# Kernel optimization log

Hardware: AMD Instinct MI355X
Metric: run time of the kernel (lower is better)

Reference implementation:

```python
import jax, jax.numpy as jnp
import numpy as np

H = 1024   # hidden_size
S = 1024   # seq_length
B = 32     # batch_size


def setup_inputs() -> dict:
    key = jax.random.key(0)
    k1, k2, k3, k4, k5, k6 = jax.random.split(key, 6)
    scale = 1.0 / np.sqrt(3 * H)
    return {
        "encoder_states": jax.random.normal(k1, (S, B, 2 * H), dtype=jnp.float32),
        "hidden": jax.random.normal(k2, (B, H), dtype=jnp.float32),
        "cell": jax.random.normal(k3, (B, H), dtype=jnp.float32),
        "W_attn": jax.random.normal(k4, (H, 3 * H), dtype=jnp.float32) * scale,
        "b_attn": jax.random.normal(k5, (H,), dtype=jnp.float32) * scale,
        "v_w": jax.random.normal(k6, (H,), dtype=jnp.float32) * (1.0 / np.sqrt(H)),
    }


def reference(encoder_states, hidden, cell, W_attn, b_attn, v_w):
    # cell is accepted by the original forward but unused.
    # Split the concat-linear into two projections (mathematically identical,
    # avoids materializing the repeated hidden + concat tensor):
    # cat((hidden_rep, enc), -1) @ W.T == hidden @ W[:, :H].T + enc @ W[:, H:].T
    W_h = W_attn[:, :H]          # [H, H]   multiplies decoder hidden
    W_e = W_attn[:, H:]          # [H, 2H]  multiplies encoder states
    enc = jnp.transpose(encoder_states, (1, 0, 2))          # [B, S, 2H]
    h_proj = hidden @ W_h.T + b_attn                         # [B, H], broadcast over S
    e_proj = jnp.einsum("bse,he->bsh", enc, W_e)             # [B, S, H]
    energy = jnp.tanh(h_proj[:, None, :] + e_proj)           # [B, S, H]
    attention = jnp.einsum("bsh,h->bs", energy, v_w)         # [B, S]
    return jax.nn.softmax(attention, axis=1)
```

## Files before the change

### kernel.cpp

```cpp
#include <hip/hip_runtime.h>

#define H 1024
#define S 1024
#define B 32
#define K2 2048

typedef unsigned short u16;
typedef __attribute__((ext_vector_type(8))) short short8;
typedef __attribute__((ext_vector_type(8))) unsigned short u16x8;
typedef __attribute__((ext_vector_type(4))) float floatx4;

__device__ __forceinline__ u16 f2bf(float f) {
  unsigned u = __float_as_uint(f);
  u += 0x7FFFu + ((u >> 16) & 1u);
  return (u16)(u >> 16);
}

__global__ void conv_enc_k(const float* __restrict__ src, u16* __restrict__ dst) {
  const int blk = blockIdx.x;
  const int s = blk >> 5, b = blk & 31;
  const int t = threadIdx.x * 8;
  const float* sp = src + (size_t)blk * K2 + t;
  u16* dp = dst + ((size_t)b * S + s) * K2 + t;
  floatx4 x = *(const floatx4*)sp;
  floatx4 y = *(const floatx4*)(sp + 4);
  u16x8 o;
  o[0] = f2bf(x[0]); o[1] = f2bf(x[1]); o[2] = f2bf(x[2]); o[3] = f2bf(x[3]);
  o[4] = f2bf(y[0]); o[5] = f2bf(y[1]); o[6] = f2bf(y[2]); o[7] = f2bf(y[3]);
  *(u16x8*)dp = o;
}

__global__ void conv_we_k(const float* __restrict__ W, u16* __restrict__ dst) {
  const int h = blockIdx.x;
  const int t = threadIdx.x * 8;
  const float* sp = W + (size_t)h * 3072 + H + t;
  u16* dp = dst + (size_t)h * K2 + t;
  floatx4 x = *(const floatx4*)sp;
  floatx4 y = *(const floatx4*)(sp + 4);
  u16x8 o;
  o[0] = f2bf(x[0]); o[1] = f2bf(x[1]); o[2] = f2bf(x[2]); o[3] = f2bf(x[3]);
  o[4] = f2bf(y[0]); o[5] = f2bf(y[1]); o[6] = f2bf(y[2]); o[7] = f2bf(y[3]);
  *(u16x8*)dp = o;
}

__global__ void hproj_k(const float* __restrict__ hidden, const float* __restrict__ W,
                        const float* __restrict__ b_attn, float* __restrict__ hp) {
  const int lane = threadIdx.x & 63;
  const int h = (blockIdx.x * blockDim.x + threadIdx.x) >> 6;
  float wr[16];
#pragma unroll
  for (int i = 0; i < 16; i++) wr[i] = W[(size_t)h * 3072 + lane + i * 64];
  for (int b = 0; b < B; b++) {
    float d = 0.f;
#pragma unroll
    for (int i = 0; i < 16; i++) d = fmaf(wr[i], hidden[b * H + lane + i * 64], d);
#pragma unroll
    for (int off = 32; off; off >>= 1) d += __shfl_xor(d, off);
    if (lane == 0) hp[b * H + h] = d + b_attn[h];
  }
}

#define BM 128
#define BN 128
#define BK 32
#define LDT 40

__global__ __launch_bounds__(256) void gemm_fused_k(
    const u16* __restrict__ A,
    const u16* __restrict__ Bw,
    const float* __restrict__ hp, const float* __restrict__ vw,
    float* __restrict__ attn) {
  __shared__ __align__(16) u16 sA[BM * LDT];
  __shared__ __align__(16) u16 sB[BN * LDT];
  const int tid = threadIdx.x;
  const int bid = blockIdx.x;
  const int ntile = bid >> 8;
  const int b = (bid & 255) >> 3;
  const int mtile = bid & 7;
  const int s0 = mtile * BM;
  const int h0 = ntile * BN;

  const int srow = tid >> 2;
  const int seg = (tid & 3) * 8;
  const u16* aG = A + ((size_t)(b * S + s0 + srow)) * K2 + seg;
  const u16* bG = Bw + ((size_t)(h0 + srow)) * K2 + seg;

  const int lane = tid & 63;
  const int wv = tid >> 6;
  const int wm = (wv >> 1) * 64;
  const int wn = (wv & 1) * 64;
  const int fr = lane & 15;
  const int kk = (lane >> 4) * 8;

  floatx4 acc[4][4];
#pragma unroll
  for (int i = 0; i < 4; i++)
#pragma unroll
    for (int j = 0; j < 4; j++) acc[i][j] = (floatx4){0.f, 0.f, 0.f, 0.f};

  for (int k0 = 0; k0 < K2; k0 += BK) {
    __syncthreads();
#pragma unroll
    for (int p = 0; p < 2; p++) {
      *(floatx4*)&sA[(srow + p * 64) * LDT + seg] =
          *(const floatx4*)(aG + (size_t)p * 64 * K2 + k0);
      *(floatx4*)&sB[(srow + p * 64) * LDT + seg] =
          *(const floatx4*)(bG + (size_t)p * 64 * K2 + k0);
    }
    __syncthreads();
    short8 af[4], bf[4];
#pragma unroll
    for (int mf = 0; mf < 4; mf++)
      af[mf] = *(const short8*)&sA[(wm + mf * 16 + fr) * LDT + kk];
#pragma unroll
    for (int nf = 0; nf < 4; nf++)
      bf[nf] = *(const short8*)&sB[(wn + nf * 16 + fr) * LDT + kk];
#pragma unroll
    for (int mf = 0; mf < 4; mf++)
#pragma unroll
      for (int nf = 0; nf < 4; nf++)
        acc[mf][nf] =
            __builtin_amdgcn_mfma_f32_16x16x32_bf16(af[mf], bf[nf], acc[mf][nf], 0, 0, 0);
  }

  const int col = fr;
  const int rgrp = lane >> 4;
  float hv[4], vv[4];
#pragma unroll
  for (int nf = 0; nf < 4; nf++) {
    const int h = h0 + wn + nf * 16 + col;
    hv[nf] = hp[b * H + h];
    vv[nf] = vw[h];
  }
#pragma unroll
  for (int mf = 0; mf < 4; mf++) {
#pragma unroll
    for (int r = 0; r < 4; r++) {
      float part = 0.f;
#pragma unroll
      for (int nf = 0; nf < 4; nf++) part += tanhf(acc[mf][nf][r] + hv[nf]) * vv[nf];
      part += __shfl_xor(part, 1);
      part += __shfl_xor(part, 2);
      part += __shfl_xor(part, 4);
      part += __shfl_xor(part, 8);
      if (col == 0)
        atomicAdd(&attn[b * S + s0 + wm + mf * 16 + rgrp * 4 + r], part);
    }
  }
}

__global__ void softmax_k(const float* __restrict__ attn, float* __restrict__ out) {
  __shared__ float red[8];
  const int b = blockIdx.x;
  const int tid = threadIdx.x;
  const float* row = attn + b * S;
  float v[4];
#pragma unroll
  for (int i = 0; i < 4; i++) v[i] = row[tid + i * 256];
  float m = fmaxf(fmaxf(v[0], v[1]), fmaxf(v[2], v[3]));
#pragma unroll
  for (int off = 32; off; off >>= 1) m = fmaxf(m, __shfl_xor(m, off));
  if ((tid & 63) == 0) red[tid >> 6] = m;
  __syncthreads();
  m = fmaxf(fmaxf(red[0], red[1]), fmaxf(red[2], red[3]));
  float e[4], sum = 0.f;
#pragma unroll
  for (int i = 0; i < 4; i++) { e[i] = __expf(v[i] - m); sum += e[i]; }
#pragma unroll
  for (int off = 32; off; off >>= 1) sum += __shfl_xor(sum, off);
  __syncthreads();
  if ((tid & 63) == 0) red[4 + (tid >> 6)] = sum;
  __syncthreads();
  sum = red[4] + red[5] + red[6] + red[7];
  const float inv = 1.0f / sum;
#pragma unroll
  for (int i = 0; i < 4; i++) out[b * S + tid + i * 256] = e[i] * inv;
}

extern "C" void kernel_launch(void* const* d_in, const int* in_sizes, int n_in,
                              void* d_out, int out_size, void* d_ws, size_t ws_size,
                              hipStream_t stream) {
  const float* enc    = (const float*)d_in[0];
  const float* hidden = (const float*)d_in[1];
  const float* W_attn = (const float*)d_in[3];
  const float* b_attn = (const float*)d_in[4];
  const float* v_w    = (const float*)d_in[5];
  float* out = (float*)d_out;

  char* ws = (char*)d_ws;
  float* attn = (float*)ws;
  float* hp   = (float*)(ws + 131072);
  u16* Web    = (u16*)(ws + 262144);
  u16* encb   = (u16*)(ws + 262144 + (size_t)H * K2 * 2);

  hipMemsetAsync(attn, 0, B * S * sizeof(float), stream);
  conv_enc_k<<<S * B, 256, 0, stream>>>(enc, encb);
  conv_we_k<<<H, 256, 0, stream>>>(W_attn, Web);
  hproj_k<<<256, 256, 0, stream>>>(hidden, W_attn, b_attn, hp);
  gemm_fused_k<<<2048, 256, 0, stream>>>(encb, Web, hp, v_w, attn);
  softmax_k<<<B, 256, 0, stream>>>(attn, out);
}
```

Measured before the change: 638.4 us.

## Use direct global-to-LDS loads with XOR swizzle in GEMM, batch enc conversion

After: 611.6 us. -4.2%, faster.

```diff
diff --git a/kernel.cpp b/kernel.cpp
--- a/kernel.cpp
+++ b/kernel.cpp
@@ -16,18 +16,28 @@
   return (u16)(u >> 16);
 }
 
+__device__ __forceinline__ void gld_lds16(const u16* g, u16* l) {
+  __builtin_amdgcn_global_load_lds(
+      (const __attribute__((address_space(1))) unsigned int*)g,
+      (__attribute__((address_space(3))) unsigned int*)l, 16, 0, 0);
+}
+
 __global__ void conv_enc_k(const float* __restrict__ src, u16* __restrict__ dst) {
-  const int blk = blockIdx.x;
-  const int s = blk >> 5, b = blk & 31;
+  const int b = blockIdx.x >> 8;
+  const int sc = blockIdx.x & 255;
   const int t = threadIdx.x * 8;
-  const float* sp = src + (size_t)blk * K2 + t;
-  u16* dp = dst + ((size_t)b * S + s) * K2 + t;
-  floatx4 x = *(const floatx4*)sp;
-  floatx4 y = *(const floatx4*)(sp + 4);
-  u16x8 o;
-  o[0] = f2bf(x[0]); o[1] = f2bf(x[1]); o[2] = f2bf(x[2]); o[3] = f2bf(x[3]);
-  o[4] = f2bf(y[0]); o[5] = f2bf(y[1]); o[6] = f2bf(y[2]); o[7] = f2bf(y[3]);
-  *(u16x8*)dp = o;
+#pragma unroll
+  for (int i = 0; i < 4; i++) {
+    const int s = sc * 4 + i;
+    const float* sp = src + ((size_t)s * B + b) * K2 + t;
+    u16* dp = dst + ((size_t)b * S + s) * K2 + t;
+    floatx4 x = *(const floatx4*)sp;
+    floatx4 y = *(const floatx4*)(sp + 4);
+    u16x8 o;
+    o[0] = f2bf(x[0]); o[1] = f2bf(x[1]); o[2] = f2bf(x[2]); o[3] = f2bf(x[3]);
+    o[4] = f2bf(y[0]); o[5] = f2bf(y[1]); o[6] = f2bf(y[2]); o[7] = f2bf(y[3]);
+    *(u16x8*)dp = o;
+  }
 }
 
 __global__ void conv_we_k(const float* __restrict__ W, u16* __restrict__ dst) {
@@ -63,15 +73,14 @@
 #define BM 128
 #define BN 128
 #define BK 32
-#define LDT 40
 
 __global__ __launch_bounds__(256) void gemm_fused_k(
     const u16* __restrict__ A,
     const u16* __restrict__ Bw,
     const float* __restrict__ hp, const float* __restrict__ vw,
     float* __restrict__ attn) {
-  __shared__ __align__(16) u16 sA[BM * LDT];
-  __shared__ __align__(16) u16 sB[BN * LDT];
+  __shared__ __align__(16) u16 sA[BM * BK];
+  __shared__ __align__(16) u16 sB[BN * BK];
   const int tid = threadIdx.x;
   const int bid = blockIdx.x;
   const int ntile = bid >> 8;
@@ -80,17 +89,18 @@
   const int s0 = mtile * BM;
   const int h0 = ntile * BN;
 
-  const int srow = tid >> 2;
-  const int seg = (tid & 3) * 8;
-  const u16* aG = A + ((size_t)(b * S + s0 + srow)) * K2 + seg;
-  const u16* bG = Bw + ((size_t)(h0 + srow)) * K2 + seg;
-
   const int lane = tid & 63;
   const int wv = tid >> 6;
   const int wm = (wv >> 1) * 64;
   const int wn = (wv & 1) * 64;
   const int fr = lane & 15;
-  const int kk = (lane >> 4) * 8;
+  const int kgrp = lane >> 4;
+
+  const int lr = lane >> 2;
+  const int sg = lane & 3;
+
+  const u16* Ab = A + (size_t)(b * S + s0) * K2;
+  const u16* Bb = Bw + (size_t)h0 * K2;
 
   floatx4 acc[4][4];
 #pragma unroll
@@ -102,19 +112,25 @@
     __syncthreads();
 #pragma unroll
     for (int p = 0; p < 2; p++) {
-      *(floatx4*)&sA[(srow + p * 64) * LDT + seg] =
-          *(const floatx4*)(aG + (size_t)p * 64 * K2 + k0);
-      *(floatx4*)&sB[(srow + p * 64) * LDT + seg] =
-          *(const floatx4*)(bG + (size_t)p * 64 * K2 + k0);
+      const int rA = wv * 32 + p * 16 + lr;
+      gld_lds16(Ab + (size_t)rA * K2 + k0 + (size_t)((sg ^ (rA & 3)) * 8),
+                &sA[(wv * 32 + p * 16) * BK]);
+      gld_lds16(Bb + (size_t)rA * K2 + k0 + (size_t)((sg ^ (rA & 3)) * 8),
+                &sB[(wv * 32 + p * 16) * BK]);
     }
     __syncthreads();
+
     short8 af[4], bf[4];
 #pragma unroll
-    for (int mf = 0; mf < 4; mf++)
-      af[mf] = *(const short8*)&sA[(wm + mf * 16 + fr) * LDT + kk];
-#pragma unroll
-    for (int nf = 0; nf < 4; nf++)
-      bf[nf] = *(const short8*)&sB[(wn + nf * 16 + fr) * LDT + kk];
+    for (int mf = 0; mf < 4; mf++) {
+      const int row = wm + mf * 16 + fr;
+      af[mf] = *(const short8*)&sA[row * BK + (kgrp ^ (row & 3)) * 8];
+    }
+#pragma unroll
+    for (int nf = 0; nf < 4; nf++) {
+      const int row = wn + nf * 16 + fr;
+      bf[nf] = *(const short8*)&sB[row * BK + (kgrp ^ (row & 3)) * 8];
+    }
 #pragma unroll
     for (int mf = 0; mf < 4; mf++)
 #pragma unroll
@@ -194,7 +210,7 @@
   u16* encb   = (u16*)(ws + 262144 + (size_t)H * K2 * 2);
 
   hipMemsetAsync(attn, 0, B * S * sizeof(float), stream);
-  conv_enc_k<<<S * B, 256, 0, stream>>>(enc, encb);
+  conv_enc_k<<<B * 256, 256, 0, stream>>>(enc, encb);
   conv_we_k<<<H, 256, 0, stream>>>(W_attn, Web);
   hproj_k<<<256, 256, 0, stream>>>(hidden, W_attn, b_attn, hp);
   gemm_fused_k<<<2048, 256, 0, stream>>>(encb, Web, hp, v_w, attn);
```
